# Optimization experiments

Hardware: AMD Instinct MI355X
Metric: run time of the kernel (lower is better)

Reference implementation:

```python
import jax, jax.numpy as jnp
import numpy as np

N, E = 50000, 640000
D_IN, D_HID, D_OUT, HEADS = 128, 128, 128, 2


def _lin_init(k, fan_in, fan_out):
    return jax.random.normal(k, (fan_in, fan_out), jnp.float32) / np.sqrt(fan_in)


def setup_inputs() -> dict:
    key = jax.random.key(0)
    ks = jax.random.split(key, 20)
    inp = {
        "x": jax.random.normal(ks[0], (N, D_IN), jnp.float32),
        "edge_index": jax.random.randint(ks[1], (2, E), 0, N, dtype=jnp.int32),
    }
    # layer 1: in -> hid (heads*per_head = 2 * 64 = 128)
    inp["Wq1"] = _lin_init(ks[2], D_IN, D_HID); inp["bq1"] = jnp.zeros((D_HID,), jnp.float32)
    inp["Wk1"] = _lin_init(ks[3], D_IN, D_HID); inp["bk1"] = jnp.zeros((D_HID,), jnp.float32)
    inp["Wv1"] = _lin_init(ks[4], D_IN, D_HID); inp["bv1"] = jnp.zeros((D_HID,), jnp.float32)
    inp["Ws1"] = _lin_init(ks[5], D_IN, D_HID); inp["bs1"] = jnp.zeros((D_HID,), jnp.float32)
    # layer 2: hid -> out
    inp["Wq2"] = _lin_init(ks[6], D_HID, D_OUT); inp["bq2"] = jnp.zeros((D_OUT,), jnp.float32)
    inp["Wk2"] = _lin_init(ks[7], D_HID, D_OUT); inp["bk2"] = jnp.zeros((D_OUT,), jnp.float32)
    inp["Wv2"] = _lin_init(ks[8], D_HID, D_OUT); inp["bv2"] = jnp.zeros((D_OUT,), jnp.float32)
    inp["Ws2"] = _lin_init(ks[9], D_HID, D_OUT); inp["bs2"] = jnp.zeros((D_OUT,), jnp.float32)
    return inp


def _transformer_conv(x, src, dst, Wq, bq, Wk, bk, Wv, bv, Ws, bs, heads):
    """PyG TransformerConv (concat=True, root_weight=True, eval mode)."""
    n = x.shape[0]
    C = Wq.shape[1] // heads  # per-head channels
    q = (x @ Wq + bq).reshape(n, heads, C)
    k = (x @ Wk + bk).reshape(n, heads, C)
    v = (x @ Wv + bv).reshape(n, heads, C)
    qi = q[dst]              # [E, H, C] gather at destination
    kj = k[src]              # [E, H, C] gather at source
    vj = v[src]              # [E, H, C]
    alpha = jnp.sum(qi * kj, axis=-1) / np.sqrt(C)   # [E, H]
    # segment softmax over incoming edges of each destination node
    amax = jax.ops.segment_max(alpha, dst, num_segments=n)   # [N, H]
    ex = jnp.exp(alpha - amax[dst])                            # [E, H]
    denom = jax.ops.segment_sum(ex, dst, num_segments=n)      # [N, H]
    a = ex / denom[dst]                                        # [E, H]
    msg = vj * a[..., None]                                    # [E, H, C]
    out = jax.ops.segment_sum(msg, dst, num_segments=n).reshape(n, heads * C)
    return out + x @ Ws + bs  # root (skip) connection


def reference(x, edge_index, Wq1, bq1, Wk1, bk1, Wv1, bv1, Ws1, bs1,
              Wq2, bq2, Wk2, bk2, Wv2, bv2, Ws2, bs2):
    src, dst = edge_index[0], edge_index[1]
    h = _transformer_conv(x, src, dst, Wq1, bq1, Wk1, bk1, Wv1, bv1, Ws1, bs1, HEADS)
    h = jax.nn.relu(h)
    return _transformer_conv(h, src, dst, Wq2, bq2, Wk2, bk2, Wv2, bv2, Ws2, bs2, HEADS)
```

## Files before the change

### kernel.cpp

```cpp
#include <hip/hip_runtime.h>
#include <math.h>

#define D 128

typedef float  f32x4  __attribute__((ext_vector_type(4)));
typedef float  f32x2  __attribute__((ext_vector_type(2)));
typedef short  bf16x8 __attribute__((ext_vector_type(8)));

__device__ inline unsigned short bf16r(float f) {
    unsigned u = __float_as_uint(f);
    u = (u + 0x7fff + ((u >> 16) & 1)) >> 16;
    return (unsigned short)u;
}
__device__ inline unsigned bf16pair(float a, float b) {
    return (unsigned)bf16r(a) | ((unsigned)bf16r(b) << 16);
}
__device__ inline float bf16lo(unsigned w) { return __uint_as_float(w << 16); }
__device__ inline float bf16hi(unsigned w) { return __uint_as_float(w & 0xffff0000u); }

__device__ inline void unpack8(uint4 w, float* f) {
    f[0] = bf16lo(w.x); f[1] = bf16hi(w.x);
    f[2] = bf16lo(w.y); f[3] = bf16hi(w.y);
    f[4] = bf16lo(w.z); f[5] = bf16hi(w.z);
    f[6] = bf16lo(w.w); f[7] = bf16hi(w.w);
}

__device__ inline unsigned pk_fp8x4(float a, float b, float c, float d) {
    unsigned w = 0;
    w = __builtin_amdgcn_cvt_pk_fp8_f32(a, b, w, false);
    w = __builtin_amdgcn_cvt_pk_fp8_f32(c, d, w, true);
    return w;
}

__device__ inline float dot8_fp8(const float* q, uint2 kw) {
    f32x2 p;
    p = __builtin_amdgcn_cvt_pk_f32_fp8((int)kw.x, false);
    float s = q[0] * p.x + q[1] * p.y;
    p = __builtin_amdgcn_cvt_pk_f32_fp8((int)kw.x, true);
    s += q[2] * p.x + q[3] * p.y;
    p = __builtin_amdgcn_cvt_pk_f32_fp8((int)kw.y, false);
    s += q[4] * p.x + q[5] * p.y;
    p = __builtin_amdgcn_cvt_pk_f32_fp8((int)kw.y, true);
    s += q[6] * p.x + q[7] * p.y;
    return s;
}

__global__ __launch_bounds__(256)
void prep(const float* __restrict__ X, unsigned* __restrict__ Xb, int npairs,
          const float* __restrict__ W0, const float* __restrict__ W1,
          const float* __restrict__ W2, const float* __restrict__ W3,
          const float* __restrict__ W4, const float* __restrict__ W5,
          const float* __restrict__ W6, const float* __restrict__ W7,
          unsigned short* __restrict__ Wt,
          int* __restrict__ cnt, int* __restrict__ bh, int* __restrict__ bcur, int n)
{
    const int nxb = (npairs + 255) >> 8;
    const int nz  = (n + 255) >> 8;
    const int b = blockIdx.x;
    if (b < nxb) {
        int i = b * 256 + threadIdx.x;
        if (i < npairs) {
            float2 v = *(const float2*)&X[2 * i];
            Xb[i] = bf16pair(v.x, v.y);
        }
    } else if (b < nxb + nz) {
        int i = (b - nxb) * 256 + threadIdx.x;
        if (i < n) cnt[i] = 0;
    } else if (b < nxb + nz + 8) {
        int wi = b - nxb - nz;
        const float* Ws[8] = {W0, W1, W2, W3, W4, W5, W6, W7};
        const float* W = Ws[wi];
        unsigned short* o = Wt + wi * 16384;
        for (int i = threadIdx.x; i < 16384; i += 256) {
            int k = i >> 7, c = i & 127;
            o[c * 128 + k] = bf16r(W[i]);
        }
    } else {
        if (threadIdx.x < 64) { bh[threadIdx.x] = 0; bcur[threadIdx.x] = 0; }
    }
}

__global__ __launch_bounds__(256)
void gemm_es(const unsigned short* __restrict__ Xb, int n,
             const unsigned short* __restrict__ Wtall,
             const float* __restrict__ bq, const float* __restrict__ bk,
             const float* __restrict__ bv, const float* __restrict__ bs,
             unsigned short* __restrict__ Qp, unsigned char* __restrict__ K8,
             unsigned short* __restrict__ Vp, unsigned short* __restrict__ Sp,
             int gemmBlocks,
             const int* __restrict__ src, const int* __restrict__ dst, int e,
             const int* __restrict__ row_ptr, const int* __restrict__ rank,
             int* __restrict__ csr_src)
{
    const int bid = blockIdx.x;
    if (bid >= gemmBlocks) {
        int i = (bid - gemmBlocks) * 256 + threadIdx.x;
        if (i < e) {
            int d = dst[i];
            csr_src[row_ptr[d] + rank[i]] = src[i];
        }
        return;
    }
    const int w = bid & 3;
    const int rowBase = (bid >> 2) * 128;
    const unsigned short* W = Wtall + w * 16384;
    const float* bias = (w == 0) ? bq : (w == 1) ? bk : (w == 2) ? bv : bs;

    __shared__ unsigned short Asm[128 * 136];

    const int tid  = threadIdx.x;
    const int wave = tid >> 6;
    const int lane = tid & 63;
    const int wr   = wave >> 1;
    const int wc   = wave & 1;
    const int q16  = lane >> 4;
    const int r16  = lane & 15;

    #pragma unroll
    for (int i = 0; i < 8; ++i) {
        int g = tid + 256 * i;
        int m = g >> 4, c = g & 15;
        int row = rowBase + m; if (row >= n) row = n - 1;
        uint4 da = *(const uint4*)(Xb + (size_t)row * 128 + c * 8);
        *(uint4*)&Asm[m * 136 + c * 8] = da;
    }

    const unsigned short* Wbase = W + (size_t)(wc * 64 + r16) * 128 + q16 * 8;
    bf16x8 bcu[4], bnx[4];
    #pragma unroll
    for (int nj = 0; nj < 4; ++nj)
        bcu[nj] = *(const bf16x8*)(Wbase + nj * 16 * 128);

    __syncthreads();

    f32x4 acc[4][4];
    #pragma unroll
    for (int mi = 0; mi < 4; ++mi)
        #pragma unroll
        for (int nj = 0; nj < 4; ++nj) acc[mi][nj] = (f32x4)(0.f);

    #pragma unroll
    for (int kc = 0; kc < 4; ++kc) {
        if (kc < 3) {
            #pragma unroll
            for (int nj = 0; nj < 4; ++nj)
                bnx[nj] = *(const bf16x8*)(Wbase + nj * 16 * 128 + (kc + 1) * 32);
        }
        bf16x8 a[4];
        #pragma unroll
        for (int mi = 0; mi < 4; ++mi)
            a[mi] = *(const bf16x8*)&Asm[(wr * 64 + mi * 16 + r16) * 136 + kc * 32 + q16 * 8];
        #pragma unroll
        for (int mi = 0; mi < 4; ++mi)
            #pragma unroll
            for (int nj = 0; nj < 4; ++nj)
                acc[mi][nj] = __builtin_amdgcn_mfma_f32_16x16x32_bf16(a[mi], bcu[nj], acc[mi][nj], 0, 0, 0);
        #pragma unroll
        for (int nj = 0; nj < 4; ++nj) bcu[nj] = bnx[nj];
    }

    __syncthreads();
    #pragma unroll
    for (int nj = 0; nj < 4; ++nj) {
        const int col = wc * 64 + nj * 16 + r16;
        const float bias_c = bias[col];
        #pragma unroll
        for (int mi = 0; mi < 4; ++mi) {
            const int rbase = wr * 64 + mi * 16 + q16 * 4;
            #pragma unroll
            for (int r = 0; r < 4; ++r)
                Asm[(rbase + r) * 132 + col] = bf16r(acc[mi][nj][r] + bias_c);
        }
    }
    __syncthreads();
    if (w == 1) {
        #pragma unroll
        for (int i = 0; i < 8; ++i) {
            int g = tid + 256 * i;
            int m = g >> 4, c = g & 15;
            int row = rowBase + m;
            if (row < n) {
                uint4 d2 = *(const uint4*)&Asm[m * 132 + c * 8];
                float f[8];
                unpack8(d2, f);
                uint2 o;
                o.x = pk_fp8x4(f[0], f[1], f[2], f[3]);
                o.y = pk_fp8x4(f[4], f[5], f[6], f[7]);
                *(uint2*)(K8 + (size_t)row * 128 + c * 8) = o;
            }
        }
    } else {
        unsigned short* plane = (w == 0) ? Qp : (w == 2) ? Vp : Sp;
        #pragma unroll
        for (int i = 0; i < 8; ++i) {
            int g = tid + 256 * i;
            int m = g >> 4, c = g & 15;
            int row = rowBase + m;
            if (row < n) {
                uint4 d2 = *(const uint4*)&Asm[m * 132 + c * 8];
                *(uint4*)(plane + (size_t)row * 128 + c * 8) = d2;
            }
        }
    }
}

__global__ void degree_hist(const int* __restrict__ dst, int e,
                            int* __restrict__ cnt, int* __restrict__ rank)
{
    int i = blockIdx.x * blockDim.x + threadIdx.x;
    if (i < e) rank[i] = atomicAdd(&cnt[dst[i]], 1);
}

__global__ __launch_bounds__(256)
void scan_hist(const int* __restrict__ cnt, int n, int* __restrict__ bsum, int* __restrict__ bh)
{
    __shared__ int sm[256];
    __shared__ int lh[64];
    if (threadIdx.x < 64) lh[threadIdx.x] = 0;
    int i = blockIdx.x * 256 + threadIdx.x;
    int v = (i < n) ? cnt[i] : 0;
    sm[threadIdx.x] = v;
    __syncthreads();
    if (i < n) atomicAdd(&lh[min(v, 63)], 1);
    #pragma unroll
    for (int off = 128; off > 0; off >>= 1) {
        if (threadIdx.x < off) sm[threadIdx.x] += sm[threadIdx.x + off];
        __syncthreads();
    }
    if (threadIdx.x == 0) bsum[blockIdx.x] = sm[0];
    if (threadIdx.x < 64 && lh[threadIdx.x] > 0)
        atomicAdd(&bh[threadIdx.x], lh[threadIdx.x]);
}

__global__ __launch_bounds__(256)
void scan2(int* __restrict__ bsum, int nb, const int* __restrict__ bh, int* __restrict__ boff)
{
    __shared__ int sm[256];
    int v = (threadIdx.x < nb) ? bsum[threadIdx.x] : 0;
    sm[threadIdx.x] = v;
    __syncthreads();
    int acc = v;
    for (int off = 1; off < 256; off <<= 1) {
        int t = (threadIdx.x >= off) ? sm[threadIdx.x - off] : 0;
        __syncthreads();
        acc += t;
        sm[threadIdx.x] = acc;
        __syncthreads();
    }
    if (threadIdx.x < nb) bsum[threadIdx.x] = acc - v;
    if (threadIdx.x == 0) {
        int run = 0;
        for (int b = 63; b >= 0; --b) { boff[b] = run; run += bh[b]; }
    }
}

__global__ __launch_bounds__(256)
void scan3_scatter(const int* __restrict__ cnt, const int* __restrict__ bsum,
                   int* __restrict__ row_ptr, int n, int e,
                   const int* __restrict__ boff, int* __restrict__ bcur,
                   int* __restrict__ perm)
{
    __shared__ int sm[256];
    __shared__ int lh[64];
    __shared__ int lbase[64];
    if (threadIdx.x < 64) lh[threadIdx.x] = 0;
    __syncthreads();
    int i = blockIdx.x * 256 + threadIdx.x;
    int v = (i < n) ? cnt[i] : 0;
    sm[threadIdx.x] = v;
    int b = 0, local = 0;
    if (i < n) {
        b = min(v, 63);
        local = atomicAdd(&lh[b], 1);
    }
    __syncthreads();
    int acc = v;
    for (int off = 1; off < 256; off <<= 1) {
        int t = (threadIdx.x >= off) ? sm[threadIdx.x - off] : 0;
        __syncthreads();
        acc += t;
        sm[threadIdx.x] = acc;
        __syncthreads();
    }
    if (i < n) row_ptr[i] = bsum[blockIdx.x] + acc - v;
    if (blockIdx.x == 0 && threadIdx.x == 0) row_ptr[n] = e;
    if (threadIdx.x < 64 && lh[threadIdx.x] > 0)
        lbase[threadIdx.x] = atomicAdd(&bcur[threadIdx.x], lh[threadIdx.x]);
    __syncthreads();
    if (i < n) perm[boff[b] + lbase[b] + local] = i;
}

__device__ inline void load4(const uint2* __restrict__ K8, const uint4* __restrict__ Vp,
                             const int* __restrict__ csr, int i, int l16,
                             uint2* k, uint4* v)
{
    int s0 = csr[i], s1 = csr[i+1], s2 = csr[i+2], s3 = csr[i+3];
    k[0] = K8[(size_t)s0 * 16 + l16];  v[0] = Vp[(size_t)s0 * 16 + l16];
    k[1] = K8[(size_t)s1 * 16 + l16];  v[1] = Vp[(size_t)s1 * 16 + l16];
    k[2] = K8[(size_t)s2 * 16 + l16];  v[2] = Vp[(size_t)s2 * 16 + l16];
    k[3] = K8[(size_t)s3 * 16 + l16];  v[3] = Vp[(size_t)s3 * 16 + l16];
}

__device__ inline void consume4(const uint2* k, const uint4* v, const float* q,
                                float& m, float& l, float* acc)
{
    float d0 = dot8_fp8(q, k[0]);
    float d1 = dot8_fp8(q, k[1]);
    float d2 = dot8_fp8(q, k[2]);
    float d3 = dot8_fp8(q, k[3]);

    d0 += __shfl_xor(d0, 4, 64); d1 += __shfl_xor(d1, 4, 64);
    d2 += __shfl_xor(d2, 4, 64); d3 += __shfl_xor(d3, 4, 64);
    d0 += __shfl_xor(d0, 2, 64); d1 += __shfl_xor(d1, 2, 64);
    d2 += __shfl_xor(d2, 2, 64); d3 += __shfl_xor(d3, 2, 64);
    d0 += __shfl_xor(d0, 1, 64); d1 += __shfl_xor(d1, 1, 64);
    d2 += __shfl_xor(d2, 1, 64); d3 += __shfl_xor(d3, 1, 64);

    float a0 = d0 * 0.125f, a1 = d1 * 0.125f, a2 = d2 * 0.125f, a3 = d3 * 0.125f;
    float m4 = fmaxf(fmaxf(a0, a1), fmaxf(a2, a3));
    float mn = fmaxf(m, m4);
    float corr = __expf(m - mn);
    float p0 = __expf(a0 - mn), p1 = __expf(a1 - mn);
    float p2 = __expf(a2 - mn), p3 = __expf(a3 - mn);
    l = l * corr + (p0 + p1 + p2 + p3);

    float v0f[8], v1f[8], v2f[8], v3f[8];
    unpack8(v[0], v0f); unpack8(v[1], v1f); unpack8(v[2], v2f); unpack8(v[3], v3f);
    #pragma unroll
    for (int c2 = 0; c2 < 8; ++c2) {
        float t = acc[c2] * corr;
        t += p0 * v0f[c2]; t += p1 * v1f[c2];
        t += p2 * v2f[c2]; t += p3 * v3f[c2];
        acc[c2] = t;
    }
    m = mn;
}

__global__ __launch_bounds__(256)
void attn(const uint4* __restrict__ Qp, const uint2* __restrict__ K8,
          const uint4* __restrict__ Vp, const uint4* __restrict__ Sp,
          const int* __restrict__ row_ptr, const int* __restrict__ csr_src,
          const int* __restrict__ perm,
          float* __restrict__ outf, uint4* __restrict__ outb,
          int n, int do_relu)
{
    const int wid  = (blockIdx.x * 256 + threadIdx.x) >> 6;
    const int lane = threadIdx.x & 63;
    const int nq   = lane >> 4;
    const int l16  = lane & 15;
    const int nidx = wid * 4 + nq;
    const int node = (nidx < n) ? perm[nidx] : -1;

    float q[8];
    float sv[8];
    int beg = 0, end = 0;
    if (node >= 0) {
        uint4 qw = Qp[(size_t)node * 16 + l16];
        unpack8(qw, q);
        unpack8(Sp[(size_t)node * 16 + l16], sv);
        beg = row_ptr[node];
        end = row_ptr[node + 1];
    }

    float m = -INFINITY, l = 0.f;
    float acc[8] = {0.f, 0.f, 0.f, 0.f, 0.f, 0.f, 0.f, 0.f};

    int i = beg;
    uint2 ka[4], kb[4];
    uint4 va[4], vb[4];
    if (i + 4 <= end) load4(K8, Vp, csr_src, i, l16, ka, va);
    while (i + 8 <= end) {
        load4(K8, Vp, csr_src, i + 4, l16, kb, vb);
        consume4(ka, va, q, m, l, acc);
        i += 4;
        if (i + 8 <= end) {
            load4(K8, Vp, csr_src, i + 4, l16, ka, va);
            consume4(kb, vb, q, m, l, acc);
            i += 4;
        } else {
            #pragma unroll
            for (int t = 0; t < 4; ++t) { ka[t] = kb[t]; va[t] = vb[t]; }
        }
    }
    if (i + 4 <= end) {
        consume4(ka, va, q, m, l, acc);
        i += 4;
    }
    while (i < end) {
        int s = csr_src[i];
        uint2 kw = K8[(size_t)s * 16 + l16];
        uint4 vw = Vp[(size_t)s * 16 + l16];
        float vf[8];
        unpack8(vw, vf);
        float part = dot8_fp8(q, kw);
        part += __shfl_xor(part, 4, 64);
        part += __shfl_xor(part, 2, 64);
        part += __shfl_xor(part, 1, 64);
        float alpha = part * 0.125f;
        float mn = fmaxf(m, alpha);
        float corr = __expf(m - mn);
        float p = __expf(alpha - mn);
        l = l * corr + p;
        #pragma unroll
        for (int c2 = 0; c2 < 8; ++c2) acc[c2] = acc[c2] * corr + p * vf[c2];
        m = mn;
        ++i;
    }

    if (node >= 0) {
        float inv = (l > 0.f) ? (1.f / l) : 0.f;
        float r[8];
        #pragma unroll
        for (int c2 = 0; c2 < 8; ++c2) r[c2] = acc[c2] * inv + sv[c2];
        if (do_relu) {
            #pragma unroll
            for (int c2 = 0; c2 < 8; ++c2) r[c2] = fmaxf(r[c2], 0.f);
        }
        if (outb) {
            uint4 o;
            o.x = bf16pair(r[0], r[1]); o.y = bf16pair(r[2], r[3]);
            o.z = bf16pair(r[4], r[5]); o.w = bf16pair(r[6], r[7]);
            outb[(size_t)node * 16 + l16] = o;
        } else {
            *(float4*)&outf[(size_t)node * 128 + l16 * 8]     = make_float4(r[0], r[1], r[2], r[3]);
            *(float4*)&outf[(size_t)node * 128 + l16 * 8 + 4] = make_float4(r[4], r[5], r[6], r[7]);
        }
    }
}

extern "C" void kernel_launch(void* const* d_in, const int* in_sizes, int n_in,
                              void* d_out, int out_size, void* d_ws, size_t ws_size,
                              hipStream_t stream)
{
    const float* x    = (const float*)d_in[0];
    const int*   edge = (const int*)d_in[1];
    const int n = in_sizes[0] / D;
    const int e = in_sizes[1] / 2;
    const int* srcv = edge;
    const int* dstv = edge + e;

    const float* Wq1 = (const float*)d_in[2];  const float* bq1 = (const float*)d_in[3];
    const float* Wk1 = (const float*)d_in[4];  const float* bk1 = (const float*)d_in[5];
    const float* Wv1 = (const float*)d_in[6];  const float* bv1 = (const float*)d_in[7];
    const float* Ws1 = (const float*)d_in[8];  const float* bs1 = (const float*)d_in[9];
    const float* Wq2 = (const float*)d_in[10]; const float* bq2 = (const float*)d_in[11];
    const float* Wk2 = (const float*)d_in[12]; const float* bk2 = (const float*)d_in[13];
    const float* Wv2 = (const float*)d_in[14]; const float* bv2 = (const float*)d_in[15];
    const float* Ws2 = (const float*)d_in[16]; const float* bs2 = (const float*)d_in[17];

    char* wsb = (char*)d_ws;
    size_t off = 0;
    auto alloc = [&](size_t bytes) -> void* {
        void* p = wsb + off;
        off += (bytes + 255) & ~(size_t)255;
        return p;
    };
    unsigned short* Qp = (unsigned short*)alloc((size_t)n * D * sizeof(unsigned short));
    unsigned char*  K8 = (unsigned char*)alloc((size_t)n * D);
    unsigned short* Vp = (unsigned short*)alloc((size_t)n * D * sizeof(unsigned short));
    unsigned short* Sp = (unsigned short*)alloc((size_t)n * D * sizeof(unsigned short));
    unsigned short* Xb = (unsigned short*)alloc((size_t)n * D * sizeof(unsigned short));
    unsigned short* Hu = (unsigned short*)alloc((size_t)n * D * sizeof(unsigned short));
    unsigned short* Wt = (unsigned short*)alloc(8 * 16384 * sizeof(unsigned short));
    int* cnt     = (int*)alloc((size_t)n * sizeof(int));
    int* row_ptr = (int*)alloc((size_t)(n + 1) * sizeof(int));
    int* bsum    = (int*)alloc(1024 * sizeof(int));
    int* perm    = (int*)alloc((size_t)n * sizeof(int));
    int* bh      = (int*)alloc(64 * sizeof(int));
    int* bcur    = (int*)alloc(64 * sizeof(int));
    int* boff    = (int*)alloc(64 * sizeof(int));
    int* rank    = (int*)alloc((size_t)e * sizeof(int));
    int* csr_src = (int*)alloc((size_t)e * sizeof(int));
    (void)ws_size; (void)n_in; (void)out_size;

    const int nb  = (n + 255) / 256;
    const int npairs = n * 64;
    const int nprep  = (npairs + 255) / 256 + nb + 8 + 1;

    prep<<<nprep, 256, 0, stream>>>(x, (unsigned*)Xb, npairs,
        Wq1, Wk1, Wv1, Ws1, Wq2, Wk2, Wv2, Ws2, Wt, cnt, bh, bcur, n);

    degree_hist<<<(e + 255) / 256, 256, 0, stream>>>(dstv, e, cnt, rank);
    scan_hist<<<nb, 256, 0, stream>>>(cnt, n, bsum, bh);
    scan2<<<1, 256, 0, stream>>>(bsum, nb, bh, boff);
    scan3_scatter<<<nb, 256, 0, stream>>>(cnt, bsum, row_ptr, n, e, boff, bcur, perm);

    const int gemmBlocks = 4 * ((n + 127) / 128);
    const int esBlocks   = (e + 255) / 256;
    const int ablocks = ((n + 3) / 4 + 3) / 4;

    gemm_es<<<gemmBlocks + esBlocks, 256, 0, stream>>>(Xb, n, Wt,
        bq1, bk1, bv1, bs1, Qp, K8, Vp, Sp, gemmBlocks,
        srcv, dstv, e, row_ptr, rank, csr_src);
    attn<<<ablocks, 256, 0, stream>>>((const uint4*)Qp, (const uint2*)K8, (const uint4*)Vp,
                                      (const uint4*)Sp, row_ptr, csr_src, perm,
                                      nullptr, (uint4*)Hu, n, 1);

    gemm_es<<<gemmBlocks, 256, 0, stream>>>(Hu, n, Wt + 4 * 16384,
        bq2, bk2, bv2, bs2, Qp, K8, Vp, Sp, gemmBlocks,
        srcv, dstv, 0, row_ptr, rank, csr_src);
    attn<<<ablocks, 256, 0, stream>>>((const uint4*)Qp, (const uint2*)K8, (const uint4*)Vp,
                                      (const uint4*)Sp, row_ptr, csr_src, perm,
                                      (float*)d_out, nullptr, n, 0);
}
```

Measured before the change: 314.9 us.

## Fuse degree histogram into prep and compute all four projections per GEMM block

The degree-histogram atomics move into the prep kernel as extra blocks, and zeroing of the count array becomes a hipMemsetAsync, removing one kernel launch. The GEMM now launches one block per 128-row tile and loops over the four weight matrices, reusing the staged input tile in shared memory instead of reloading it four times, with a separate output staging buffer. This cuts input reads and launch count, but gives four times fewer GEMM blocks with more serial work each, about 68KB of shared memory per block (lower occupancy), and histogram atomics that now run alongside the conversion work.

```diff
diff --git a/kernel.cpp b/kernel.cpp
--- a/kernel.cpp
+++ b/kernel.cpp
@@ -52,10 +52,10 @@
           const float* __restrict__ W4, const float* __restrict__ W5,
           const float* __restrict__ W6, const float* __restrict__ W7,
           unsigned short* __restrict__ Wt,
-          int* __restrict__ cnt, int* __restrict__ bh, int* __restrict__ bcur, int n)
+          int* __restrict__ cnt, int* __restrict__ bh, int* __restrict__ bcur,
+          const int* __restrict__ dstv, int e, int* __restrict__ rank)
 {
     const int nxb = (npairs + 255) >> 8;
-    const int nz  = (n + 255) >> 8;
     const int b = blockIdx.x;
     if (b < nxb) {
         int i = b * 256 + threadIdx.x;
@@ -63,11 +63,8 @@
             float2 v = *(const float2*)&X[2 * i];
             Xb[i] = bf16pair(v.x, v.y);
         }
-    } else if (b < nxb + nz) {
-        int i = (b - nxb) * 256 + threadIdx.x;
-        if (i < n) cnt[i] = 0;
-    } else if (b < nxb + nz + 8) {
-        int wi = b - nxb - nz;
+    } else if (b < nxb + 8) {
+        int wi = b - nxb;
         const float* Ws[8] = {W0, W1, W2, W3, W4, W5, W6, W7};
         const float* W = Ws[wi];
         unsigned short* o = Wt + wi * 16384;
@@ -75,8 +72,11 @@
             int k = i >> 7, c = i & 127;
             o[c * 128 + k] = bf16r(W[i]);
         }
+    } else if (b == nxb + 8) {
+        if (threadIdx.x < 64) { bh[threadIdx.x] = 0; bcur[threadIdx.x] = 0; }
     } else {
-        if (threadIdx.x < 64) { bh[threadIdx.x] = 0; bcur[threadIdx.x] = 0; }
+        int i = (b - nxb - 9) * 256 + threadIdx.x;
+        if (i < e) rank[i] = atomicAdd(&cnt[dstv[i]], 1);
     }
 }
 
@@ -101,12 +101,10 @@
         }
         return;
     }
-    const int w = bid & 3;
-    const int rowBase = (bid >> 2) * 128;
-    const unsigned short* W = Wtall + w * 16384;
-    const float* bias = (w == 0) ? bq : (w == 1) ? bk : (w == 2) ? bv : bs;
+    const int rowBase = bid * 128;
 
     __shared__ unsigned short Asm[128 * 136];
+    __shared__ unsigned short Csm[128 * 132];
 
     const int tid  = threadIdx.x;
     const int wave = tid >> 6;
@@ -124,91 +122,88 @@
         uint4 da = *(const uint4*)(Xb + (size_t)row * 128 + c * 8);
         *(uint4*)&Asm[m * 136 + c * 8] = da;
     }
-
-    const unsigned short* Wbase = W + (size_t)(wc * 64 + r16) * 128 + q16 * 8;
-    bf16x8 bcu[4], bnx[4];
-    #pragma unroll
-    for (int nj = 0; nj < 4; ++nj)
-        bcu[nj] = *(const bf16x8*)(Wbase + nj * 16 * 128);
-
     __syncthreads();
 
-    f32x4 acc[4][4];
-    #pragma unroll
-    for (int mi = 0; mi < 4; ++mi)
-        #pragma unroll
-        for (int nj = 0; nj < 4; ++nj) acc[mi][nj] = (f32x4)(0.f);
-
-    #pragma unroll
-    for (int kc = 0; kc < 4; ++kc) {
-        if (kc < 3) {
-            #pragma unroll
-            for (int nj = 0; nj < 4; ++nj)
-                bnx[nj] = *(const bf16x8*)(Wbase + nj * 16 * 128 + (kc + 1) * 32);
-        }
-        bf16x8 a[4];
+    for (int w = 0; w < 4; ++w) {
+        const unsigned short* W = Wtall + w * 16384;
+        const float* bias = (w == 0) ? bq : (w == 1) ? bk : (w == 2) ? bv : bs;
+        const unsigned short* Wbase = W + (size_t)(wc * 64 + r16) * 128 + q16 * 8;
+
+        f32x4 acc[4][4];
         #pragma unroll
         for (int mi = 0; mi < 4; ++mi)
-            a[mi] = *(const bf16x8*)&Asm[(wr * 64 + mi * 16 + r16) * 136 + kc * 32 + q16 * 8];
+            #pragma unroll
+            for (int nj = 0; nj < 4; ++nj) acc[mi][nj] = (f32x4)(0.f);
+
+        bf16x8 bcu[4], bnx[4];
         #pragma unroll
-        for (int mi = 0; mi < 4; ++mi)
-            #pragma unroll
-            for (int nj = 0; nj < 4; ++nj)
-                acc[mi][nj] = __builtin_amdgcn_mfma_f32_16x16x32_bf16(a[mi], bcu[nj], acc[mi][nj], 0, 0, 0);
+        for (int nj = 0; nj < 4; ++nj)
+            bcu[nj] = *(const bf16x8*)(Wbase + nj * 16 * 128);
+
         #pragma unroll
-        for (int nj = 0; nj < 4; ++nj) bcu[nj] = bnx[nj];
-    }
-
-    __syncthreads();
-    #pragma unroll
-    for (int nj = 0; nj < 4; ++nj) {
-        const int col = wc * 64 + nj * 16 + r16;
-        const float bias_c = bias[col];
+        for (int kc = 0; kc < 4; ++kc) {
+            if (kc < 3) {
+                #pragma unroll
+                for (int nj = 0; nj < 4; ++nj)
+                    bnx[nj] = *(const bf16x8*)(Wbase + nj * 16 * 128 + (kc + 1) * 32);
+            }
+            bf16x8 a[4];
+            #pragma unroll
+            for (int mi = 0; mi < 4; ++mi)
+                a[mi] = *(const bf16x8*)&Asm[(wr * 64 + mi * 16 + r16) * 136 + kc * 32 + q16 * 8];
+            #pragma unroll
+            for (int mi = 0; mi < 4; ++mi)
+                #pragma unroll
+                for (int nj = 0; nj < 4; ++nj)
+                    acc[mi][nj] = __builtin_amdgcn_mfma_f32_16x16x32_bf16(a[mi], bcu[nj], acc[mi][nj], 0, 0, 0);
+            #pragma unroll
+            for (int nj = 0; nj < 4; ++nj) bcu[nj] = bnx[nj];
+        }
+
+        __syncthreads();
         #pragma unroll
-        for (int mi = 0; mi < 4; ++mi) {
-            const int rbase = wr * 64 + mi * 16 + q16 * 4;
-            #pragma unroll
-            for (int r = 0; r < 4; ++r)
-                Asm[(rbase + r) * 132 + col] = bf16r(acc[mi][nj][r] + bias_c);
-        }
-    }
-    __syncthreads();
-    if (w == 1) {
-        #pragma unroll
-        for (int i = 0; i < 8; ++i) {
-            int g = tid + 256 * i;
-            int m = g >> 4, c = g & 15;
-            int row = rowBase + m;
-            if (row < n) {
-                uint4 d2 = *(const uint4*)&Asm[m * 132 + c * 8];
-                float f[8];
-                unpack8(d2, f);
-                uint2 o;
-                o.x = pk_fp8x4(f[0], f[1], f[2], f[3]);
-                o.y = pk_fp8x4(f[4], f[5], f[6], f[7]);
-                *(uint2*)(K8 + (size_t)row * 128 + c * 8) = o;
+        for (int nj = 0; nj < 4; ++nj) {
+            const int col = wc * 64 + nj * 16 + r16;
+            const float bias_c = bias[col];
+            #pragma unroll
+            for (int mi = 0; mi < 4; ++mi) {
+                const int rbase = wr * 64 + mi * 16 + q16 * 4;
+                #pragma unroll
+                for (int r = 0; r < 4; ++r)
+                    Csm[(rbase + r) * 132 + col] = bf16r(acc[mi][nj][r] + bias_c);
             }
         }
-    } else {
-        unsigned short* plane = (w == 0) ? Qp : (w == 2) ? Vp : Sp;
-        #pragma unroll
-        for (int i = 0; i < 8; ++i) {
-            int g = tid + 256 * i;
-            int m = g >> 4, c = g & 15;
-            int row = rowBase + m;
-            if (row < n) {
-                uint4 d2 = *(const uint4*)&Asm[m * 132 + c * 8];
-                *(uint4*)(plane + (size_t)row * 128 + c * 8) = d2;
+        __syncthreads();
+        if (w == 1) {
+            #pragma unroll
+            for (int i = 0; i < 8; ++i) {
+                int g = tid + 256 * i;
+                int m = g >> 4, c = g & 15;
+                int row = rowBase + m;
+                if (row < n) {
+                    uint4 d2 = *(const uint4*)&Csm[m * 132 + c * 8];
+                    float f[8];
+                    unpack8(d2, f);
+                    uint2 o;
+                    o.x = pk_fp8x4(f[0], f[1], f[2], f[3]);
+                    o.y = pk_fp8x4(f[4], f[5], f[6], f[7]);
+                    *(uint2*)(K8 + (size_t)row * 128 + c * 8) = o;
+                }
             }
-        }
-    }
-}
-
-__global__ void degree_hist(const int* __restrict__ dst, int e,
-                            int* __restrict__ cnt, int* __restrict__ rank)
-{
-    int i = blockIdx.x * blockDim.x + threadIdx.x;
-    if (i < e) rank[i] = atomicAdd(&cnt[dst[i]], 1);
+        } else {
+            unsigned short* plane = (w == 0) ? Qp : (w == 2) ? Vp : Sp;
+            #pragma unroll
+            for (int i = 0; i < 8; ++i) {
+                int g = tid + 256 * i;
+                int m = g >> 4, c = g & 15;
+                int row = rowBase + m;
+                if (row < n) {
+                    uint4 d2 = *(const uint4*)&Csm[m * 132 + c * 8];
+                    *(uint4*)(plane + (size_t)row * 128 + c * 8) = d2;
+                }
+            }
+        }
+    }
 }
 
 __global__ __launch_bounds__(256)
@@ -475,21 +470,22 @@
 
     const int nb  = (n + 255) / 256;
     const int npairs = n * 64;
-    const int nprep  = (npairs + 255) / 256 + nb + 8 + 1;
-
+    const int eb  = (e + 255) / 256;
+    const int nprep = (npairs + 255) / 256 + 8 + 1 + eb;
+
+    hipMemsetAsync(cnt, 0, (size_t)n * sizeof(int), stream);
     prep<<<nprep, 256, 0, stream>>>(x, (unsigned*)Xb, npairs,
-        Wq1, Wk1, Wv1, Ws1, Wq2, Wk2, Wv2, Ws2, Wt, cnt, bh, bcur, n);
-
-    degree_hist<<<(e + 255) / 256, 256, 0, stream>>>(dstv, e, cnt, rank);
+        Wq1, Wk1, Wv1, Ws1, Wq2, Wk2, Wv2, Ws2, Wt, cnt, bh, bcur,
+        dstv, e, rank);
+
     scan_hist<<<nb, 256, 0, stream>>>(cnt, n, bsum, bh);
     scan2<<<1, 256, 0, stream>>>(bsum, nb, bh, boff);
     scan3_scatter<<<nb, 256, 0, stream>>>(cnt, bsum, row_ptr, n, e, boff, bcur, perm);
 
-    const int gemmBlocks = 4 * ((n + 127) / 128);
-    const int esBlocks   = (e + 255) / 256;
+    const int gemmBlocks = (n + 127) / 128;
     const int ablocks = ((n + 3) / 4 + 3) / 4;
 
-    gemm_es<<<gemmBlocks + esBlocks, 256, 0, stream>>>(Xb, n, Wt,
+    gemm_es<<<gemmBlocks + eb, 256, 0, stream>>>(Xb, n, Wt,
         bq1, bk1, bv1, bs1, Qp, K8, Vp, Sp, gemmBlocks,
         srcv, dstv, e, row_ptr, rank, csr_src);
     attn<<<ablocks, 256, 0, stream>>>((const uint4*)Qp, (const uint2*)K8, (const uint4*)Vp,
```

Result: faster. 301.1 us (-4.4%).
